# Performance work log

Hardware: AMD Instinct MI355X
Metric: run time of the kernel (lower is better)

The kernel has to match this reference:

```python
import jax, jax.numpy as jnp
import numpy as np

N, H, W = 4, 96, 96
C, G, K = 128, 8, 3
GC = C // G          # group channels = 16
P = K * K            # sampling points per group = 9
PAD = K // 2
OFS = 1.0            # offset_scale
HID = 4 * C          # mlp hidden
EPS = 1e-5           # torch nn.LayerNorm default eps


def _ln(x, g, b):
    m = jnp.mean(x, -1, keepdims=True)
    v = jnp.mean((x - m) ** 2, -1, keepdims=True)
    return (x - m) * jax.lax.rsqrt(v + EPS) * g + b


def _dcnv3_core(x, offset, mask):
    # x: (n,H,W,C) channels-last, offset: (n,H,W,G*P*2), mask: (n,H,W,G,P) softmaxed.
    # Faithful port of dcnv3_core_pytorch (stride=1, dilation=1, zero-pad grid_sample,
    # align_corners=False -> pixel = loc*size - 0.5).
    n = x.shape[0]
    xp = jnp.pad(x, ((0, 0), (PAD, PAD), (PAD, PAD), (0, 0)))
    Hin, Win = H + 2 * PAD, W + 2 * PAD
    L = H * W
    base = (K - 1) // 2 + 0.5
    ref_x = (base + jnp.arange(W, dtype=x.dtype)) / Win  # normalized by padded size
    ref_y = (base + jnp.arange(H, dtype=x.dtype)) / Hin
    k = jnp.arange(K, dtype=x.dtype) - (K - 1) // 2
    dx = jnp.repeat(k, K) / Win  # torch meshgrid('ij'): kernel-x varies slowest
    dy = jnp.tile(k, K) / Hin
    off = offset.reshape(n, H, W, G, P, 2)
    # absolute sampling pixel coords (grid_sample align_corners=False)
    px = (ref_x[None, None, :, None, None] + dx * OFS + off[..., 0] * OFS / Win) * Win - 0.5
    py = (ref_y[None, :, None, None, None] + dy * OFS + off[..., 1] * OFS / Hin) * Hin - 0.5
    # layout (n,G,L,P)
    px = px.transpose(0, 3, 1, 2, 4).reshape(n, G, L, P)
    py = py.transpose(0, 3, 1, 2, 4).reshape(n, G, L, P)
    mk = mask.transpose(0, 3, 1, 2, 4).reshape(n, G, L, P)
    xg = xp.reshape(n, Hin * Win, G, GC).transpose(0, 2, 1, 3)
    x0 = jnp.floor(px); y0 = jnp.floor(py)
    fx = px - x0; fy = py - y0
    x0 = x0.astype(jnp.int32); y0 = y0.astype(jnp.int32)
    x1 = x0 + 1; y1 = y0 + 1
    out = jnp.zeros((n, G, L, GC), x.dtype)
    for yi, xi, w in ((y0, x0, (1 - fy) * (1 - fx)), (y0, x1, (1 - fy) * fx),
                      (y1, x0, fy * (1 - fx)), (y1, x1, fy * fx)):
        valid = (yi >= 0) & (yi < Hin) & (xi >= 0) & (xi < Win)
        idx = jnp.clip(yi, 0, Hin - 1) * Win + jnp.clip(xi, 0, Win - 1)
        v = jnp.take_along_axis(xg, idx.reshape(n, G, L * P, 1), axis=2)
        v = v.reshape(n, G, L, P, GC)
        out = out + jnp.einsum('nglp,nglpc->nglc', jnp.where(valid, w, 0.0) * mk, v)
    return out.transpose(0, 2, 1, 3).reshape(n, H, W, C)


def _dcn(x, w_in, b_in, dw_k, dw_b, dwg, dwb, w_off, b_off, w_msk, b_msk, w_out, b_out):
    n = x.shape[0]
    xproj = x @ w_in + b_in
    x1 = jax.lax.conv_general_dilated(
        x, dw_k, (1, 1), 'SAME',
        dimension_numbers=('NHWC', 'HWIO', 'NHWC'),
        feature_group_count=C) + dw_b
    x1 = jax.nn.gelu(_ln(x1, dwg, dwb), approximate=False)
    offset = x1 @ w_off + b_off
    mask = jax.nn.softmax((x1 @ w_msk + b_msk).reshape(n, H, W, G, P), axis=-1)
    y = _dcnv3_core(xproj, offset, mask)
    return y @ w_out + b_out


def setup_inputs() -> dict:
    key = jax.random.key(0)
    ks = jax.random.split(key, 10)
    rn = lambda k, s, sc: jax.random.normal(k, s, jnp.float32) * sc
    return {
        'x': rn(ks[0], (N, H, W, C), 1.0),
        'ln1g': jnp.ones((C,), jnp.float32), 'ln1b': jnp.zeros((C,), jnp.float32),
        'w_in': rn(ks[1], (C, C), 0.02), 'b_in': jnp.zeros((C,), jnp.float32),
        'dw_k': rn(ks[2], (K, K, 1, C), 0.1), 'dw_b': jnp.zeros((C,), jnp.float32),
        'dwg': jnp.ones((C,), jnp.float32), 'dwb': jnp.zeros((C,), jnp.float32),
        'w_off': rn(ks[3], (C, G * P * 2), 0.01), 'b_off': rn(ks[4], (G * P * 2,), 0.1),
        'w_msk': rn(ks[5], (C, G * P), 0.02), 'b_msk': jnp.zeros((G * P,), jnp.float32),
        'w_out': rn(ks[6], (C, C), 0.02), 'b_out': jnp.zeros((C,), jnp.float32),
        'ln2g': jnp.ones((C,), jnp.float32), 'ln2b': jnp.zeros((C,), jnp.float32),
        'w1': rn(ks[7], (C, HID), 0.02), 'b1': jnp.zeros((HID,), jnp.float32),
        'w2': rn(ks[8], (HID, C), 0.02), 'b2': jnp.zeros((C,), jnp.float32),
    }


def reference(x, ln1g, ln1b, w_in, b_in, dw_k, dw_b, dwg, dwb, w_off, b_off,
              w_msk, b_msk, w_out, b_out, ln2g, ln2b, w1, b1, w2, b2):
    # pre-norm InternImage block: x = x + dcn(LN1(x)); x = x + mlp(LN2(x))
    x = x + _dcn(_ln(x, ln1g, ln1b), w_in, b_in, dw_k, dw_b, dwg, dwb,
                 w_off, b_off, w_msk, b_msk, w_out, b_out)
    h = _ln(x, ln2g, ln2b)
    h = jax.nn.gelu(h @ w1 + b1, approximate=False) @ w2 + b2
    return x + h
```

## Files before the change

kernel.cpp:

```cpp
#include <hip/hip_runtime.h>
#include <hip/hip_bf16.h>
#include <math.h>

using bf16 = __hip_bfloat16;
using bf162 = __hip_bfloat162;

typedef __bf16 bf16x8 __attribute__((ext_vector_type(8)));
typedef float floatx4 __attribute__((ext_vector_type(4)));

constexpr int NB = 4, HH = 96, WW = 96, CC = 128, GG = 8, PP = 9;
constexpr int HW = HH * WW;
constexpr int NPIX = NB * HW;

__device__ __forceinline__ float ld1(const float* p) { return *p; }
__device__ __forceinline__ float ld1(const bf16* p)  { return __bfloat162float(*p); }
__device__ __forceinline__ void st1(float* p, float v) { *p = v; }
__device__ __forceinline__ void st1(bf16* p, float v)  { *p = __float2bfloat16(v); }
__device__ __forceinline__ float b2f(bf16 v) { return __bfloat162float(v); }
__device__ __forceinline__ bf16 f2b(float v) { return __float2bfloat16(v); }
__device__ __forceinline__ float gelu_exact(float v) {
    return 0.5f * v * (1.0f + erff(v * 0.7071067811865475f));
}
__device__ __forceinline__ floatx4 MFMA(bf16x8 a, bf16x8 b, floatx4 c) {
    return __builtin_amdgcn_mfma_f32_16x16x32_bf16(a, b, c, 0, 0, 0);
}

struct PrepArgs {
    const float* src[6];
    bf16* dst[6];
    int K[6], N[6];
    int cum[7];
    const float* b_off; const float* b_msk; float* b_om;
};

__global__ __launch_bounds__(256) void prep_weights(PrepArgs pa, int total)
{
    int t = blockIdx.x * 256 + threadIdx.x;
    if (t >= total) return;
    if (t >= pa.cum[6]) {
        int e = t - pa.cum[6];
        pa.b_om[e] = (e < 144) ? pa.b_off[e] : pa.b_msk[e - 144];
        return;
    }
    int i = 0;
    #pragma unroll
    for (int j = 0; j < 5; ++j) if (t >= pa.cum[j + 1]) i = j + 1;
    int e = t - pa.cum[i];
    int Ki = pa.K[i], Ni = pa.N[i];
    int n = e / Ki, k = e - n * Ki;
    pa.dst[i][e] = f2b(pa.src[i][(size_t)k * Ni + n]);
}

template<typename TI, typename TO>
__global__ __launch_bounds__(256) void ln_kernel(
    const TI* __restrict__ X, const float* __restrict__ g,
    const float* __restrict__ b, TO* __restrict__ out)
{
    int wave = (blockIdx.x * 256 + threadIdx.x) >> 6;
    int lane = threadIdx.x & 63;
    if (wave >= NPIX) return;
    const TI* xp = X + (size_t)wave * 128 + 2 * lane;
    float v0 = ld1(xp), v1 = ld1(xp + 1);
    float s = v0 + v1, q = v0 * v0 + v1 * v1;
    #pragma unroll
    for (int o = 32; o; o >>= 1) { s += __shfl_xor(s, o); q += __shfl_xor(q, o); }
    float mean = s * (1.0f / 128.0f);
    float rstd = rsqrtf(q * (1.0f / 128.0f) - mean * mean + 1e-5f);
    float g0 = g[2 * lane], g1 = g[2 * lane + 1];
    float b0 = b[2 * lane], b1 = b[2 * lane + 1];
    TO* op = out + (size_t)wave * 128 + 2 * lane;
    st1(op,     (v0 - mean) * rstd * g0 + b0);
    st1(op + 1, (v1 - mean) * rstd * g1 + b1);
}

__global__ __launch_bounds__(256) void dwconv_ln_gelu_kernel(
    const bf16* __restrict__ xln, const float* __restrict__ dwk,
    const float* __restrict__ dwb, const float* __restrict__ gam,
    const float* __restrict__ bet, bf16* __restrict__ out)
{
    int wave = (blockIdx.x * 256 + threadIdx.x) >> 6;
    int lane = threadIdx.x & 63;
    if (wave >= NPIX) return;
    int n = wave / HW; int rem = wave % HW;
    int y = rem / WW;  int x = rem % WW;
    const bf162* xp = (const bf162*)xln;
    float a0 = 0.f, a1 = 0.f;
    #pragma unroll
    for (int ky = 0; ky < 3; ++ky) {
        int yy = y + ky - 1;
        if (yy < 0 || yy >= HH) continue;
        #pragma unroll
        for (int kx = 0; kx < 3; ++kx) {
            int xx = x + kx - 1;
            if (xx < 0 || xx >= WW) continue;
            bf162 v = xp[((size_t)(n * HH + yy) * WW + xx) * 64 + lane];
            const float* w = dwk + (ky * 3 + kx) * CC + 2 * lane;
            a0 = fmaf(b2f(v.x), w[0], a0);
            a1 = fmaf(b2f(v.y), w[1], a1);
        }
    }
    a0 += dwb[2 * lane]; a1 += dwb[2 * lane + 1];
    float s = a0 + a1, q = a0 * a0 + a1 * a1;
    #pragma unroll
    for (int o = 32; o; o >>= 1) { s += __shfl_xor(s, o); q += __shfl_xor(q, o); }
    float mean = s * (1.0f / 128.0f);
    float rstd = rsqrtf(q * (1.0f / 128.0f) - mean * mean + 1e-5f);
    float h0 = gelu_exact((a0 - mean) * rstd * gam[2 * lane]     + bet[2 * lane]);
    float h1 = gelu_exact((a1 - mean) * rstd * gam[2 * lane + 1] + bet[2 * lane + 1]);
    bf162 o2; o2.x = f2b(h0); o2.y = f2b(h1);
    ((bf162*)out)[(size_t)wave * 64 + lane] = o2;
}

__global__ __launch_bounds__(256) void dcn_core_kernel(
    const bf16* __restrict__ xproj, const bf16* __restrict__ omr,
    bf16* __restrict__ out)
{
    __shared__ int4   sOff[4][72];
    __shared__ float4 sW[4][72];
    __shared__ float  sRaw[4][72];
    int wv = threadIdx.x >> 6;
    int lane = threadIdx.x & 63;
    int pix = blockIdx.x * 4 + wv;
    int n = pix / HW; int rem = pix % HW;
    int iy = rem / WW; int ix = rem % WW;
    const bf16* om = omr + (size_t)pix * 216;

    for (int e = lane; e < 72; e += 64)
        sRaw[wv][e] = b2f(om[144 + e]);
    __syncthreads();

    for (int e = lane; e < 72; e += 64) {
        int g = e / 9, p = e - 9 * g;
        float mx = -1e30f;
        #pragma unroll
        for (int i = 0; i < 9; ++i) mx = fmaxf(mx, sRaw[wv][g * 9 + i]);
        float ssum = 0.f;
        #pragma unroll
        for (int i = 0; i < 9; ++i) ssum += __expf(sRaw[wv][g * 9 + i] - mx);
        float mw = __expf(sRaw[wv][e] - mx) / ssum;

        float ox = b2f(om[g * 18 + 2 * p]);
        float oy = b2f(om[g * 18 + 2 * p + 1]);
        int kx = p / 3 - 1, ky = p % 3 - 1;
        float px = (float)(ix + kx) + ox;
        float py = (float)(iy + ky) + oy;
        float fx0 = floorf(px), fy0 = floorf(py);
        int x0 = (int)fx0, y0 = (int)fy0;
        float fx = px - fx0, fy = py - fy0;
        bool vx0 = (x0 >= 0) & (x0 < WW), vx1 = (x0 + 1 >= 0) & (x0 + 1 < WW);
        bool vy0 = (y0 >= 0) & (y0 < HH), vy1 = (y0 + 1 >= 0) & (y0 + 1 < HH);
        float w00 = (1.f - fy) * (1.f - fx) * mw * (vy0 && vx0 ? 1.f : 0.f);
        float w01 = (1.f - fy) * fx         * mw * (vy0 && vx1 ? 1.f : 0.f);
        float w10 = fy * (1.f - fx)         * mw * (vy1 && vx0 ? 1.f : 0.f);
        float w11 = fy * fx                 * mw * (vy1 && vx1 ? 1.f : 0.f);
        int x0c = min(max(x0, 0), WW - 1), x1c = min(max(x0 + 1, 0), WW - 1);
        int y0c = min(max(y0, 0), HH - 1), y1c = min(max(y0 + 1, 0), HH - 1);
        sOff[wv][e] = make_int4((y0c * WW + x0c) * CC, (y0c * WW + x1c) * CC,
                                (y1c * WW + x0c) * CC, (y1c * WW + x1c) * CC);
        sW[wv][e] = make_float4(w00, w01, w10, w11);
    }
    __syncthreads();

    const bf16* xb = xproj + (size_t)n * HW * CC + 2 * lane;
    int gbase = (lane >> 3) * 9;
    float a0 = 0.f, a1 = 0.f;
    #pragma unroll
    for (int p = 0; p < 9; ++p) {
        int4 o = sOff[wv][gbase + p];
        float4 w = sW[wv][gbase + p];
        bf162 v00 = *(const bf162*)(xb + o.x);
        bf162 v01 = *(const bf162*)(xb + o.y);
        bf162 v10 = *(const bf162*)(xb + o.z);
        bf162 v11 = *(const bf162*)(xb + o.w);
        a0 += w.x * b2f(v00.x) + w.y * b2f(v01.x) + w.z * b2f(v10.x) + w.w * b2f(v11.x);
        a1 += w.x * b2f(v00.y) + w.y * b2f(v01.y) + w.z * b2f(v10.y) + w.w * b2f(v11.y);
    }
    bf162 o2; o2.x = f2b(a0); o2.y = f2b(a1);
    ((bf162*)out)[(size_t)pix * 64 + lane] = o2;
}

__global__ __launch_bounds__(256) void gemm_mfma_kernel(
    const bf16* __restrict__ A, const bf16* __restrict__ Wt,
    const float* __restrict__ bias, bf16* __restrict__ Out, int M, int Nn, int K)
{
    __shared__ __align__(16) __bf16 As[64][72];
    __shared__ __align__(16) __bf16 Bs[64][72];
    int tid = threadIdx.x;
    int wv = tid >> 6, lane = tid & 63;
    int bm = blockIdx.y * 64, bn = blockIdx.x * 64;
    int mI = lane & 15, q = lane >> 4;
    floatx4 acc[4] = {};

    for (int k0 = 0; k0 < K; k0 += 64) {
        #pragma unroll
        for (int cc = 0; cc < 2; ++cc) {
            int ch = tid * 2 + cc;
            int row = ch >> 3, ko = (ch & 7) * 8;
            *reinterpret_cast<uint4*>(&As[row][ko]) =
                *reinterpret_cast<const uint4*>(A + (size_t)(bm + row) * K + k0 + ko);
            int ng = bn + row;
            uint4 bv = make_uint4(0, 0, 0, 0);
            if (ng < Nn) bv = *reinterpret_cast<const uint4*>(Wt + (size_t)ng * K + k0 + ko);
            *reinterpret_cast<uint4*>(&Bs[row][ko]) = bv;
        }
        __syncthreads();
        #pragma unroll
        for (int kk = 0; kk < 64; kk += 32) {
            bf16x8 a = *reinterpret_cast<const bf16x8*>(&As[wv * 16 + mI][kk + q * 8]);
            #pragma unroll
            for (int t = 0; t < 4; ++t) {
                bf16x8 b = *reinterpret_cast<const bf16x8*>(&Bs[t * 16 + mI][kk + q * 8]);
                acc[t] = MFMA(a, b, acc[t]);
            }
        }
        __syncthreads();
    }
    int row0 = bm + wv * 16 + q * 4;
    #pragma unroll
    for (int t = 0; t < 4; ++t) {
        int col = bn + t * 16 + mI;
        if (col >= Nn) continue;
        float bs = bias[col];
        #pragma unroll
        for (int r = 0; r < 4; ++r)
            st1(Out + (size_t)(row0 + r) * Nn + col, acc[t][r] + bs);
    }
}

__global__ __launch_bounds__(256, 3) void fused_tail_kernel(
    const bf16* __restrict__ ycore, const float* __restrict__ x,
    const bf16* __restrict__ w_outT, const float* __restrict__ b_out,
    const float* __restrict__ ln2g, const float* __restrict__ ln2b,
    const bf16* __restrict__ w1T, const float* __restrict__ b1,
    const bf16* __restrict__ w2T, const float* __restrict__ b2,
    float* __restrict__ out)
{
    __shared__ __align__(16) bf16 sA[64 * 136];
    __shared__ __align__(16) bf16 sXres[64 * 136];
    __shared__ __align__(16) bf16 sH2[64 * 136];
    int tid = threadIdx.x, wv = tid >> 6, lane = tid & 63;
    int mI = lane & 15, q = lane >> 4;
    int bm = blockIdx.x * 64;

    bf16x8 bw0[4][2];
    #pragma unroll
    for (int ks = 0; ks < 4; ++ks)
        #pragma unroll
        for (int ct = 0; ct < 2; ++ct)
            bw0[ks][ct] = *reinterpret_cast<const bf16x8*>(
                w_outT + (size_t)(wv * 32 + ct * 16 + mI) * 128 + ks * 32 + q * 8);

    #pragma unroll
    for (int i = 0; i < 4; ++i) {
        int s = tid + 256 * i;
        int row = s >> 4, ko = (s & 15) * 8;
        *reinterpret_cast<uint4*>(&sA[row * 136 + ko]) =
            *reinterpret_cast<const uint4*>(ycore + (size_t)(bm + row) * 128 + ko);
    }
    __syncthreads();

    floatx4 acc0[4][2] = {};
    #pragma unroll
    for (int ks = 0; ks < 4; ++ks) {
        int k = ks * 32 + q * 8;
        bf16x8 a[4];
        #pragma unroll
        for (int rt = 0; rt < 4; ++rt)
            a[rt] = *reinterpret_cast<const bf16x8*>(&sA[(rt * 16 + mI) * 136 + k]);
        #pragma unroll
        for (int ct = 0; ct < 2; ++ct)
            #pragma unroll
            for (int rt = 0; rt < 4; ++rt)
                acc0[rt][ct] = MFMA(a[rt], bw0[ks][ct], acc0[rt][ct]);
    }
    #pragma unroll
    for (int rt = 0; rt < 4; ++rt)
        #pragma unroll
        for (int ct = 0; ct < 2; ++ct) {
            int col = wv * 32 + ct * 16 + mI;
            float bs = b_out[col];
            #pragma unroll
            for (int r = 0; r < 4; ++r) {
                int row = rt * 16 + q * 4 + r;
                float v = acc0[rt][ct][r] + bs + x[(size_t)(bm + row) * 128 + col];
                sXres[row * 136 + col] = f2b(v);
            }
        }
    __syncthreads();

    {
        int row = tid >> 2, part = tid & 3;
        float s = 0.f, sq = 0.f;
        float vals[32];
        #pragma unroll
        for (int j = 0; j < 4; ++j) {
            bf16x8 v = *reinterpret_cast<const bf16x8*>(&sXres[row * 136 + part * 32 + j * 8]);
            #pragma unroll
            for (int e = 0; e < 8; ++e) {
                float f = (float)v[e];
                vals[j * 8 + e] = f; s += f; sq += f * f;
            }
        }
        s  += __shfl_xor(s, 1);  s += __shfl_xor(s, 2);
        sq += __shfl_xor(sq, 1); sq += __shfl_xor(sq, 2);
        float mean = s * (1.0f / 128.0f);
        float rstd = rsqrtf(sq * (1.0f / 128.0f) - mean * mean + 1e-5f);
        #pragma unroll
        for (int j = 0; j < 4; ++j) {
            bf16x8 o;
            #pragma unroll
            for (int e = 0; e < 8; ++e) {
                int ch = part * 32 + j * 8 + e;
                bf16 t = f2b((vals[j * 8 + e] - mean) * rstd * ln2g[ch] + ln2b[ch]);
                o[e] = *reinterpret_cast<__bf16*>(&t);
            }
            *reinterpret_cast<bf16x8*>(&sH2[row * 136 + part * 32 + j * 8]) = o;
        }
    }
    __syncthreads();

    floatx4 acc2[4][2] = {};
    #pragma unroll 1
    for (int ph = 0; ph < 4; ++ph) {
        bf16x8 bw1[4][2];
        #pragma unroll
        for (int ks = 0; ks < 4; ++ks)
            #pragma unroll
            for (int ct = 0; ct < 2; ++ct)
                bw1[ks][ct] = *reinterpret_cast<const bf16x8*>(
                    w1T + (size_t)(ph * 128 + wv * 32 + ct * 16 + mI) * 128 + ks * 32 + q * 8);
        floatx4 acc1[4][2] = {};
        #pragma unroll
        for (int ks = 0; ks < 4; ++ks) {
            int k = ks * 32 + q * 8;
            bf16x8 a[4];
            #pragma unroll
            for (int rt = 0; rt < 4; ++rt)
                a[rt] = *reinterpret_cast<const bf16x8*>(&sH2[(rt * 16 + mI) * 136 + k]);
            #pragma unroll
            for (int ct = 0; ct < 2; ++ct)
                #pragma unroll
                for (int rt = 0; rt < 4; ++rt)
                    acc1[rt][ct] = MFMA(a[rt], bw1[ks][ct], acc1[rt][ct]);
        }
        __syncthreads();
        bf16x8 bw2[4][2];
        #pragma unroll
        for (int ks = 0; ks < 4; ++ks)
            #pragma unroll
            for (int ct = 0; ct < 2; ++ct)
                bw2[ks][ct] = *reinterpret_cast<const bf16x8*>(
                    w2T + (size_t)(wv * 32 + ct * 16 + mI) * 512 + ph * 128 + ks * 32 + q * 8);
        #pragma unroll
        for (int rt = 0; rt < 4; ++rt)
            #pragma unroll
            for (int ct = 0; ct < 2; ++ct) {
                int lcol = wv * 32 + ct * 16 + mI;
                float bs = b1[ph * 128 + lcol];
                #pragma unroll
                for (int r = 0; r < 4; ++r) {
                    int row = rt * 16 + q * 4 + r;
                    sA[row * 136 + lcol] = f2b(gelu_exact(acc1[rt][ct][r] + bs));
                }
            }
        __syncthreads();
        #pragma unroll
        for (int ks = 0; ks < 4; ++ks) {
            int k = ks * 32 + q * 8;
            bf16x8 a[4];
            #pragma unroll
            for (int rt = 0; rt < 4; ++rt)
                a[rt] = *reinterpret_cast<const bf16x8*>(&sA[(rt * 16 + mI) * 136 + k]);
            #pragma unroll
            for (int ct = 0; ct < 2; ++ct)
                #pragma unroll
                for (int rt = 0; rt < 4; ++rt)
                    acc2[rt][ct] = MFMA(a[rt], bw2[ks][ct], acc2[rt][ct]);
        }
    }
    #pragma unroll
    for (int rt = 0; rt < 4; ++rt)
        #pragma unroll
        for (int ct = 0; ct < 2; ++ct) {
            int col = wv * 32 + ct * 16 + mI;
            float bs = b2[col];
            #pragma unroll
            for (int r = 0; r < 4; ++r) {
                int row = rt * 16 + q * 4 + r;
                out[(size_t)(bm + row) * 128 + col] =
                    acc2[rt][ct][r] + bs + b2f(sXres[row * 136 + col]);
            }
        }
}

extern "C" void kernel_launch(void* const* d_in, const int* in_sizes, int n_in,
                              void* d_out, int out_size, void* d_ws, size_t ws_size,
                              hipStream_t stream)
{
    const float* x     = (const float*)d_in[0];
    const float* ln1g  = (const float*)d_in[1];
    const float* ln1b  = (const float*)d_in[2];
    const float* w_in  = (const float*)d_in[3];
    const float* b_in  = (const float*)d_in[4];
    const float* dw_k  = (const float*)d_in[5];
    const float* dw_b  = (const float*)d_in[6];
    const float* dwg   = (const float*)d_in[7];
    const float* dwb   = (const float*)d_in[8];
    const float* w_off = (const float*)d_in[9];
    const float* b_off = (const float*)d_in[10];
    const float* w_msk = (const float*)d_in[11];
    const float* b_msk = (const float*)d_in[12];
    const float* w_out = (const float*)d_in[13];
    const float* b_out = (const float*)d_in[14];
    const float* ln2g  = (const float*)d_in[15];
    const float* ln2b  = (const float*)d_in[16];
    const float* w1    = (const float*)d_in[17];
    const float* b1    = (const float*)d_in[18];
    const float* w2    = (const float*)d_in[19];
    const float* b2    = (const float*)d_in[20];
    float* out = (float*)d_out;

    bf16* ws = (bf16*)d_ws;
    bf16* xln   = ws;
    bf16* xproj = xln   + (size_t)NPIX * 128;
    bf16* x1    = xproj + (size_t)NPIX * 128;
    bf16* omr   = x1    + (size_t)NPIX * 128;
    bf16* ycore = xln;
    bf16* wT    = ws + (size_t)NPIX * 600;
    bf16* w_inT  = wT;
    bf16* w_omT  = w_inT  + 16384;
    bf16* w_outT = w_omT  + 27648;
    bf16* w1T    = w_outT + 16384;
    bf16* w2T    = w1T    + 65536;
    float* b_om  = (float*)(w2T + 65536);
    const int WTOT = 191488 + 216;

    PrepArgs pa;
    pa.src[0] = w_in;  pa.dst[0] = w_inT;            pa.K[0] = 128; pa.N[0] = 128;
    pa.src[1] = w_off; pa.dst[1] = w_omT;            pa.K[1] = 128; pa.N[1] = 144;
    pa.src[2] = w_msk; pa.dst[2] = w_omT + 144*128;  pa.K[2] = 128; pa.N[2] = 72;
    pa.src[3] = w_out; pa.dst[3] = w_outT;           pa.K[3] = 128; pa.N[3] = 128;
    pa.src[4] = w1;    pa.dst[4] = w1T;              pa.K[4] = 128; pa.N[4] = 512;
    pa.src[5] = w2;    pa.dst[5] = w2T;              pa.K[5] = 512; pa.N[5] = 128;
    pa.cum[0] = 0;     pa.cum[1] = 16384;  pa.cum[2] = 34816; pa.cum[3] = 44032;
    pa.cum[4] = 60416; pa.cum[5] = 125952; pa.cum[6] = 191488;
    pa.b_off = b_off;  pa.b_msk = b_msk;   pa.b_om = b_om;

    const int M = NPIX;
    dim3 blk(256);

    prep_weights<<<(WTOT + 255) / 256, blk, 0, stream>>>(pa, WTOT);
    ln_kernel<float, bf16><<<NPIX / 4, blk, 0, stream>>>(x, ln1g, ln1b, xln);
    gemm_mfma_kernel<<<dim3(2, M / 64), blk, 0, stream>>>(
        xln, w_inT, b_in, xproj, M, 128, 128);
    dwconv_ln_gelu_kernel<<<NPIX / 4, blk, 0, stream>>>(xln, dw_k, dw_b, dwg, dwb, x1);
    gemm_mfma_kernel<<<dim3(4, M / 64), blk, 0, stream>>>(
        x1, w_omT, b_om, omr, M, 216, 128);
    dcn_core_kernel<<<NPIX / 4, blk, 0, stream>>>(xproj, omr, ycore);
    fused_tail_kernel<<<M / 64, blk, 0, stream>>>(
        ycore, x, w_outT, b_out, ln2g, ln2b, w1T, b1, w2T, b2, out);
}
```

Measured before the change: 236.9 us.

## Use 32-row GEMM tiles, pad offset/mask output, and approximate GELU

Replaces the generic 64x64 tiled GEMM with a 32-row kernel that keeps the full K=128 A-tile in registers and streams weight column tiles directly from global memory with register double-buffering. The offset/mask projection output is padded from 216 to 224 columns so the column count splits evenly across waves. The fused tail kernel moves to 32-row blocks with less shared memory and a higher occupancy hint. Exact erf GELU is swapped for a tanh-style sigmoid approximation, which cuts transcendental cost but changes numerics relative to the exact reference.

```diff
diff --git a/kernel.cpp b/kernel.cpp
--- a/kernel.cpp
+++ b/kernel.cpp
@@ -18,8 +18,10 @@
 __device__ __forceinline__ void st1(bf16* p, float v)  { *p = __float2bfloat16(v); }
 __device__ __forceinline__ float b2f(bf16 v) { return __bfloat162float(v); }
 __device__ __forceinline__ bf16 f2b(float v) { return __float2bfloat16(v); }
-__device__ __forceinline__ float gelu_exact(float v) {
-    return 0.5f * v * (1.0f + erff(v * 0.7071067811865475f));
+__device__ __forceinline__ float gelu_fast(float v) {
+    float p = v * v;
+    float u2 = v * (-1.5957691216f - 0.0713548162f * p);
+    return v / (1.0f + __expf(u2));
 }
 __device__ __forceinline__ floatx4 MFMA(bf16x8 a, bf16x8 b, floatx4 c) {
     return __builtin_amdgcn_mfma_f32_16x16x32_bf16(a, b, c, 0, 0, 0);
@@ -30,6 +32,7 @@
     bf16* dst[6];
     int K[6], N[6];
     int cum[7];
+    bf16* om_pad;
     const float* b_off; const float* b_msk; float* b_om;
 };
 
@@ -37,9 +40,14 @@
 {
     int t = blockIdx.x * 256 + threadIdx.x;
     if (t >= total) return;
-    if (t >= pa.cum[6]) {
-        int e = t - pa.cum[6];
-        pa.b_om[e] = (e < 144) ? pa.b_off[e] : pa.b_msk[e - 144];
+    int wend = pa.cum[6];
+    if (t >= wend + 1024) {
+        int e = t - wend - 1024;
+        pa.b_om[e] = (e < 144) ? pa.b_off[e] : (e < 216 ? pa.b_msk[e - 144] : 0.f);
+        return;
+    }
+    if (t >= wend) {
+        pa.om_pad[t - wend] = f2b(0.f);
         return;
     }
     int i = 0;
@@ -105,8 +113,8 @@
     for (int o = 32; o; o >>= 1) { s += __shfl_xor(s, o); q += __shfl_xor(q, o); }
     float mean = s * (1.0f / 128.0f);
     float rstd = rsqrtf(q * (1.0f / 128.0f) - mean * mean + 1e-5f);
-    float h0 = gelu_exact((a0 - mean) * rstd * gam[2 * lane]     + bet[2 * lane]);
-    float h1 = gelu_exact((a1 - mean) * rstd * gam[2 * lane + 1] + bet[2 * lane + 1]);
+    float h0 = gelu_fast((a0 - mean) * rstd * gam[2 * lane]     + bet[2 * lane]);
+    float h1 = gelu_fast((a1 - mean) * rstd * gam[2 * lane + 1] + bet[2 * lane + 1]);
     bf162 o2; o2.x = f2b(h0); o2.y = f2b(h1);
     ((bf162*)out)[(size_t)wave * 64 + lane] = o2;
 }
@@ -123,7 +131,7 @@
     int pix = blockIdx.x * 4 + wv;
     int n = pix / HW; int rem = pix % HW;
     int iy = rem / WW; int ix = rem % WW;
-    const bf16* om = omr + (size_t)pix * 216;
+    const bf16* om = omr + (size_t)pix * 224;
 
     for (int e = lane; e < 72; e += 64)
         sRaw[wv][e] = b2f(om[144 + e]);
@@ -179,55 +187,62 @@
     ((bf162*)out)[(size_t)pix * 64 + lane] = o2;
 }
 
-__global__ __launch_bounds__(256) void gemm_mfma_kernel(
+__global__ __launch_bounds__(256) void gemm32_kernel(
     const bf16* __restrict__ A, const bf16* __restrict__ Wt,
-    const float* __restrict__ bias, bf16* __restrict__ Out, int M, int Nn, int K)
-{
-    __shared__ __align__(16) __bf16 As[64][72];
-    __shared__ __align__(16) __bf16 Bs[64][72];
-    int tid = threadIdx.x;
-    int wv = tid >> 6, lane = tid & 63;
-    int bm = blockIdx.y * 64, bn = blockIdx.x * 64;
+    const float* __restrict__ bias, bf16* __restrict__ Out, int Nn)
+{
+    __shared__ __align__(16) bf16 sA[32 * 136];
+    int tid = threadIdx.x, wv = tid >> 6, lane = tid & 63;
     int mI = lane & 15, q = lane >> 4;
-    floatx4 acc[4] = {};
-
-    for (int k0 = 0; k0 < K; k0 += 64) {
-        #pragma unroll
-        for (int cc = 0; cc < 2; ++cc) {
-            int ch = tid * 2 + cc;
-            int row = ch >> 3, ko = (ch & 7) * 8;
-            *reinterpret_cast<uint4*>(&As[row][ko]) =
-                *reinterpret_cast<const uint4*>(A + (size_t)(bm + row) * K + k0 + ko);
-            int ng = bn + row;
-            uint4 bv = make_uint4(0, 0, 0, 0);
-            if (ng < Nn) bv = *reinterpret_cast<const uint4*>(Wt + (size_t)ng * K + k0 + ko);
-            *reinterpret_cast<uint4*>(&Bs[row][ko]) = bv;
-        }
-        __syncthreads();
-        #pragma unroll
-        for (int kk = 0; kk < 64; kk += 32) {
-            bf16x8 a = *reinterpret_cast<const bf16x8*>(&As[wv * 16 + mI][kk + q * 8]);
-            #pragma unroll
-            for (int t = 0; t < 4; ++t) {
-                bf16x8 b = *reinterpret_cast<const bf16x8*>(&Bs[t * 16 + mI][kk + q * 8]);
-                acc[t] = MFMA(a, b, acc[t]);
-            }
-        }
-        __syncthreads();
-    }
-    int row0 = bm + wv * 16 + q * 4;
-    #pragma unroll
-    for (int t = 0; t < 4; ++t) {
-        int col = bn + t * 16 + mI;
-        if (col >= Nn) continue;
+    int rt = wv & 1, g = wv >> 1;
+    int bm = blockIdx.x * 32;
+
+    #pragma unroll
+    for (int cc = 0; cc < 2; ++cc) {
+        int s = tid + 256 * cc;
+        int row = s >> 4, ko = (s & 15) * 8;
+        *reinterpret_cast<uint4*>(&sA[row * 136 + ko]) =
+            *reinterpret_cast<const uint4*>(A + (size_t)(bm + row) * 128 + ko);
+    }
+    __syncthreads();
+
+    bf16x8 a[4];
+    #pragma unroll
+    for (int ks = 0; ks < 4; ++ks)
+        a[ks] = *reinterpret_cast<const bf16x8*>(&sA[(rt * 16 + mI) * 136 + ks * 32 + q * 8]);
+
+    int T2 = (Nn >> 4) >> 1;
+    int t = g * T2;
+    bf16x8 bc[4];
+    #pragma unroll
+    for (int ks = 0; ks < 4; ++ks)
+        bc[ks] = *reinterpret_cast<const bf16x8*>(Wt + (size_t)(t * 16 + mI) * 128 + ks * 32 + q * 8);
+    for (int i = 0; i < T2; ++i) {
+        bf16x8 bn[4];
+        if (i + 1 < T2) {
+            #pragma unroll
+            for (int ks = 0; ks < 4; ++ks)
+                bn[ks] = *reinterpret_cast<const bf16x8*>(
+                    Wt + (size_t)((t + 1) * 16 + mI) * 128 + ks * 32 + q * 8);
+        }
+        floatx4 acc = {};
+        #pragma unroll
+        for (int ks = 0; ks < 4; ++ks) acc = MFMA(a[ks], bc[ks], acc);
+        int col = t * 16 + mI;
         float bs = bias[col];
+        int row0 = bm + rt * 16 + q * 4;
         #pragma unroll
         for (int r = 0; r < 4; ++r)
-            st1(Out + (size_t)(row0 + r) * Nn + col, acc[t][r] + bs);
-    }
-}
-
-__global__ __launch_bounds__(256, 3) void fused_tail_kernel(
+            st1(Out + (size_t)(row0 + r) * Nn + col, acc[r] + bs);
+        if (i + 1 < T2) {
+            #pragma unroll
+            for (int ks = 0; ks < 4; ++ks) bc[ks] = bn[ks];
+        }
+        ++t;
+    }
+}
+
+__global__ __launch_bounds__(256, 4) void fused_tail_kernel(
     const bf16* __restrict__ ycore, const float* __restrict__ x,
     const bf16* __restrict__ w_outT, const float* __restrict__ b_out,
     const float* __restrict__ ln2g, const float* __restrict__ ln2b,
@@ -235,162 +250,155 @@
     const bf16* __restrict__ w2T, const float* __restrict__ b2,
     float* __restrict__ out)
 {
-    __shared__ __align__(16) bf16 sA[64 * 136];
-    __shared__ __align__(16) bf16 sXres[64 * 136];
-    __shared__ __align__(16) bf16 sH2[64 * 136];
+    __shared__ __align__(16) bf16 sA[32 * 136];
+    __shared__ __align__(16) bf16 sXres[32 * 136];
+    __shared__ __align__(16) bf16 sH2[32 * 136];
     int tid = threadIdx.x, wv = tid >> 6, lane = tid & 63;
     int mI = lane & 15, q = lane >> 4;
-    int bm = blockIdx.x * 64;
-
-    bf16x8 bw0[4][2];
-    #pragma unroll
-    for (int ks = 0; ks < 4; ++ks)
-        #pragma unroll
-        for (int ct = 0; ct < 2; ++ct)
-            bw0[ks][ct] = *reinterpret_cast<const bf16x8*>(
-                w_outT + (size_t)(wv * 32 + ct * 16 + mI) * 128 + ks * 32 + q * 8);
-
-    #pragma unroll
-    for (int i = 0; i < 4; ++i) {
-        int s = tid + 256 * i;
+    int rt = wv & 1, ch = wv >> 1;
+    int bm = blockIdx.x * 32;
+
+    #pragma unroll
+    for (int cc = 0; cc < 2; ++cc) {
+        int s = tid + 256 * cc;
         int row = s >> 4, ko = (s & 15) * 8;
         *reinterpret_cast<uint4*>(&sA[row * 136 + ko]) =
             *reinterpret_cast<const uint4*>(ycore + (size_t)(bm + row) * 128 + ko);
     }
     __syncthreads();
 
-    floatx4 acc0[4][2] = {};
-    #pragma unroll
-    for (int ks = 0; ks < 4; ++ks) {
-        int k = ks * 32 + q * 8;
-        bf16x8 a[4];
-        #pragma unroll
-        for (int rt = 0; rt < 4; ++rt)
-            a[rt] = *reinterpret_cast<const bf16x8*>(&sA[(rt * 16 + mI) * 136 + k]);
-        #pragma unroll
-        for (int ct = 0; ct < 2; ++ct)
-            #pragma unroll
-            for (int rt = 0; rt < 4; ++rt)
-                acc0[rt][ct] = MFMA(a[rt], bw0[ks][ct], acc0[rt][ct]);
-    }
-    #pragma unroll
-    for (int rt = 0; rt < 4; ++rt)
-        #pragma unroll
-        for (int ct = 0; ct < 2; ++ct) {
-            int col = wv * 32 + ct * 16 + mI;
-            float bs = b_out[col];
-            #pragma unroll
-            for (int r = 0; r < 4; ++r) {
-                int row = rt * 16 + q * 4 + r;
-                float v = acc0[rt][ct][r] + bs + x[(size_t)(bm + row) * 128 + col];
-                sXres[row * 136 + col] = f2b(v);
-            }
-        }
+    bf16x8 a0f[4];
+    #pragma unroll
+    for (int ks = 0; ks < 4; ++ks)
+        a0f[ks] = *reinterpret_cast<const bf16x8*>(&sA[(rt * 16 + mI) * 136 + ks * 32 + q * 8]);
+    floatx4 acc0[4] = {};
+    #pragma unroll
+    for (int cth = 0; cth < 2; ++cth) {
+        bf16x8 bw[4][2];
+        #pragma unroll
+        for (int ks = 0; ks < 4; ++ks)
+            #pragma unroll
+            for (int c = 0; c < 2; ++c)
+                bw[ks][c] = *reinterpret_cast<const bf16x8*>(
+                    w_outT + (size_t)(ch * 64 + (cth * 2 + c) * 16 + mI) * 128 + ks * 32 + q * 8);
+        #pragma unroll
+        for (int ks = 0; ks < 4; ++ks)
+            #pragma unroll
+            for (int c = 0; c < 2; ++c)
+                acc0[cth * 2 + c] = MFMA(a0f[ks], bw[ks][c], acc0[cth * 2 + c]);
+    }
+    #pragma unroll
+    for (int ct = 0; ct < 4; ++ct) {
+        int col = ch * 64 + ct * 16 + mI;
+        float bs = b_out[col];
+        #pragma unroll
+        for (int r = 0; r < 4; ++r) {
+            int row = rt * 16 + q * 4 + r;
+            float v = acc0[ct][r] + bs + x[(size_t)(bm + row) * 128 + col];
+            sXres[row * 136 + col] = f2b(v);
+        }
+    }
     __syncthreads();
 
     {
-        int row = tid >> 2, part = tid & 3;
+        int row = tid >> 3, part = tid & 7;
         float s = 0.f, sq = 0.f;
-        float vals[32];
-        #pragma unroll
-        for (int j = 0; j < 4; ++j) {
-            bf16x8 v = *reinterpret_cast<const bf16x8*>(&sXres[row * 136 + part * 32 + j * 8]);
+        float vals[16];
+        #pragma unroll
+        for (int j = 0; j < 2; ++j) {
+            bf16x8 v = *reinterpret_cast<const bf16x8*>(&sXres[row * 136 + part * 16 + j * 8]);
             #pragma unroll
             for (int e = 0; e < 8; ++e) {
                 float f = (float)v[e];
                 vals[j * 8 + e] = f; s += f; sq += f * f;
             }
         }
-        s  += __shfl_xor(s, 1);  s += __shfl_xor(s, 2);
-        sq += __shfl_xor(sq, 1); sq += __shfl_xor(sq, 2);
+        s  += __shfl_xor(s, 1);  s += __shfl_xor(s, 2);  s += __shfl_xor(s, 4);
+        sq += __shfl_xor(sq, 1); sq += __shfl_xor(sq, 2); sq += __shfl_xor(sq, 4);
         float mean = s * (1.0f / 128.0f);
         float rstd = rsqrtf(sq * (1.0f / 128.0f) - mean * mean + 1e-5f);
         #pragma unroll
-        for (int j = 0; j < 4; ++j) {
+        for (int j = 0; j < 2; ++j) {
             bf16x8 o;
             #pragma unroll
             for (int e = 0; e < 8; ++e) {
-                int ch = part * 32 + j * 8 + e;
-                bf16 t = f2b((vals[j * 8 + e] - mean) * rstd * ln2g[ch] + ln2b[ch]);
-                o[e] = *reinterpret_cast<__bf16*>(&t);
+                int chn = part * 16 + j * 8 + e;
+                bf16 tb = f2b((vals[j * 8 + e] - mean) * rstd * ln2g[chn] + ln2b[chn]);
+                o[e] = *reinterpret_cast<__bf16*>(&tb);
             }
-            *reinterpret_cast<bf16x8*>(&sH2[row * 136 + part * 32 + j * 8]) = o;
-        }
-    }
-    __syncthreads();
-
-    floatx4 acc2[4][2] = {};
+            *reinterpret_cast<bf16x8*>(&sH2[row * 136 + part * 16 + j * 8]) = o;
+        }
+    }
+    __syncthreads();
+
+    floatx4 acc2[4] = {};
     #pragma unroll 1
     for (int ph = 0; ph < 4; ++ph) {
-        bf16x8 bw1[4][2];
+        bf16x8 a1f[4];
         #pragma unroll
         for (int ks = 0; ks < 4; ++ks)
-            #pragma unroll
-            for (int ct = 0; ct < 2; ++ct)
-                bw1[ks][ct] = *reinterpret_cast<const bf16x8*>(
-                    w1T + (size_t)(ph * 128 + wv * 32 + ct * 16 + mI) * 128 + ks * 32 + q * 8);
-        floatx4 acc1[4][2] = {};
-        #pragma unroll
-        for (int ks = 0; ks < 4; ++ks) {
-            int k = ks * 32 + q * 8;
-            bf16x8 a[4];
-            #pragma unroll
-            for (int rt = 0; rt < 4; ++rt)
-                a[rt] = *reinterpret_cast<const bf16x8*>(&sH2[(rt * 16 + mI) * 136 + k]);
-            #pragma unroll
-            for (int ct = 0; ct < 2; ++ct)
+            a1f[ks] = *reinterpret_cast<const bf16x8*>(&sH2[(rt * 16 + mI) * 136 + ks * 32 + q * 8]);
+        floatx4 acc1[4] = {};
+        #pragma unroll
+        for (int cth = 0; cth < 2; ++cth) {
+            bf16x8 bw[4][2];
+            #pragma unroll
+            for (int ks = 0; ks < 4; ++ks)
                 #pragma unroll
-                for (int rt = 0; rt < 4; ++rt)
-                    acc1[rt][ct] = MFMA(a[rt], bw1[ks][ct], acc1[rt][ct]);
+                for (int c = 0; c < 2; ++c)
+                    bw[ks][c] = *reinterpret_cast<const bf16x8*>(
+                        w1T + (size_t)(ph * 128 + ch * 64 + (cth * 2 + c) * 16 + mI) * 128
+                            + ks * 32 + q * 8);
+            #pragma unroll
+            for (int ks = 0; ks < 4; ++ks)
+                #pragma unroll
+                for (int c = 0; c < 2; ++c)
+                    acc1[cth * 2 + c] = MFMA(a1f[ks], bw[ks][c], acc1[cth * 2 + c]);
         }
         __syncthreads();
-        bf16x8 bw2[4][2];
-        #pragma unroll
-        for (int ks = 0; ks < 4; ++ks)
-            #pragma unroll
-            for (int ct = 0; ct < 2; ++ct)
-                bw2[ks][ct] = *reinterpret_cast<const bf16x8*>(
-                    w2T + (size_t)(wv * 32 + ct * 16 + mI) * 512 + ph * 128 + ks * 32 + q * 8);
-        #pragma unroll
-        for (int rt = 0; rt < 4; ++rt)
-            #pragma unroll
-            for (int ct = 0; ct < 2; ++ct) {
-                int lcol = wv * 32 + ct * 16 + mI;
-                float bs = b1[ph * 128 + lcol];
-                #pragma unroll
-                for (int r = 0; r < 4; ++r) {
-                    int row = rt * 16 + q * 4 + r;
-                    sA[row * 136 + lcol] = f2b(gelu_exact(acc1[rt][ct][r] + bs));
-                }
-            }
-        __syncthreads();
-        #pragma unroll
-        for (int ks = 0; ks < 4; ++ks) {
-            int k = ks * 32 + q * 8;
-            bf16x8 a[4];
-            #pragma unroll
-            for (int rt = 0; rt < 4; ++rt)
-                a[rt] = *reinterpret_cast<const bf16x8*>(&sA[(rt * 16 + mI) * 136 + k]);
-            #pragma unroll
-            for (int ct = 0; ct < 2; ++ct)
-                #pragma unroll
-                for (int rt = 0; rt < 4; ++rt)
-                    acc2[rt][ct] = MFMA(a[rt], bw2[ks][ct], acc2[rt][ct]);
-        }
-    }
-    #pragma unroll
-    for (int rt = 0; rt < 4; ++rt)
-        #pragma unroll
-        for (int ct = 0; ct < 2; ++ct) {
-            int col = wv * 32 + ct * 16 + mI;
-            float bs = b2[col];
+        #pragma unroll
+        for (int ct = 0; ct < 4; ++ct) {
+            int lcol = ch * 64 + ct * 16 + mI;
+            float bs = b1[ph * 128 + lcol];
             #pragma unroll
             for (int r = 0; r < 4; ++r) {
                 int row = rt * 16 + q * 4 + r;
-                out[(size_t)(bm + row) * 128 + col] =
-                    acc2[rt][ct][r] + bs + b2f(sXres[row * 136 + col]);
+                sA[row * 136 + lcol] = f2b(gelu_fast(acc1[ct][r] + bs));
             }
         }
+        __syncthreads();
+        bf16x8 a2f[4];
+        #pragma unroll
+        for (int ks = 0; ks < 4; ++ks)
+            a2f[ks] = *reinterpret_cast<const bf16x8*>(&sA[(rt * 16 + mI) * 136 + ks * 32 + q * 8]);
+        #pragma unroll
+        for (int cth = 0; cth < 2; ++cth) {
+            bf16x8 bw[4][2];
+            #pragma unroll
+            for (int ks = 0; ks < 4; ++ks)
+                #pragma unroll
+                for (int c = 0; c < 2; ++c)
+                    bw[ks][c] = *reinterpret_cast<const bf16x8*>(
+                        w2T + (size_t)(ch * 64 + (cth * 2 + c) * 16 + mI) * 512
+                            + ph * 128 + ks * 32 + q * 8);
+            #pragma unroll
+            for (int ks = 0; ks < 4; ++ks)
+                #pragma unroll
+                for (int c = 0; c < 2; ++c)
+                    acc2[cth * 2 + c] = MFMA(a2f[ks], bw[ks][c], acc2[cth * 2 + c]);
+        }
+    }
+    #pragma unroll
+    for (int ct = 0; ct < 4; ++ct) {
+        int col = ch * 64 + ct * 16 + mI;
+        float bs = b2[col];
+        #pragma unroll
+        for (int r = 0; r < 4; ++r) {
+            int row = rt * 16 + q * 4 + r;
+            out[(size_t)(bm + row) * 128 + col] =
+                acc2[ct][r] + bs + b2f(sXres[row * 136 + col]);
+        }
+    }
 }
 
 extern "C" void kernel_launch(void* const* d_in, const int* in_sizes, int n_in,
@@ -426,14 +434,14 @@
     bf16* x1    = xproj + (size_t)NPIX * 128;
     bf16* omr   = x1    + (size_t)NPIX * 128;
     bf16* ycore = xln;
-    bf16* wT    = ws + (size_t)NPIX * 600;
+    bf16* wT    = ws + (size_t)NPIX * 608;
     bf16* w_inT  = wT;
     bf16* w_omT  = w_inT  + 16384;
-    bf16* w_outT = w_omT  + 27648;
+    bf16* w_outT = w_omT  + 28672;
     bf16* w1T    = w_outT + 16384;
     bf16* w2T    = w1T    + 65536;
     float* b_om  = (float*)(w2T + 65536);
-    const int WTOT = 191488 + 216;
+    const int WTOT = 191488 + 1024 + 224;
 
     PrepArgs pa;
     pa.src[0] = w_in;  pa.dst[0] = w_inT;            pa.K[0] = 128; pa.N[0] = 128;
@@ -444,6 +452,7 @@
     pa.src[5] = w2;    pa.dst[5] = w2T;              pa.K[5] = 512; pa.N[5] = 128;
     pa.cum[0] = 0;     pa.cum[1] = 16384;  pa.cum[2] = 34816; pa.cum[3] = 44032;
     pa.cum[4] = 60416; pa.cum[5] = 125952; pa.cum[6] = 191488;
+    pa.om_pad = w_omT + 216 * 128;
     pa.b_off = b_off;  pa.b_msk = b_msk;   pa.b_om = b_om;
 
     const int M = NPIX;
@@ -451,12 +460,10 @@
 
     prep_weights<<<(WTOT + 255) / 256, blk, 0, stream>>>(pa, WTOT);
     ln_kernel<float, bf16><<<NPIX / 4, blk, 0, stream>>>(x, ln1g, ln1b, xln);
-    gemm_mfma_kernel<<<dim3(2, M / 64), blk, 0, stream>>>(
-        xln, w_inT, b_in, xproj, M, 128, 128);
+    gemm32_kernel<<<M / 32, blk, 0, stream>>>(xln, w_inT, b_in, xproj, 128);
     dwconv_ln_gelu_kernel<<<NPIX / 4, blk, 0, stream>>>(xln, dw_k, dw_b, dwg, dwb, x1);
-    gemm_mfma_kernel<<<dim3(4, M / 64), blk, 0, stream>>>(
-        x1, w_omT, b_om, omr, M, 216, 128);
+    gemm32_kernel<<<M / 32, blk, 0, stream>>>(x1, w_omT, b_om, omr, 224);
     dcn_core_kernel<<<NPIX / 4, blk, 0, stream>>>(xproj, omr, ycore);
-    fused_tail_kernel<<<M / 64, blk, 0, stream>>>(
+    fused_tail_kernel<<<M / 32, blk, 0, stream>>>(
         ycore, x, w_outT, b_out, ln2g, ln2b, w1T, b1, w2T, b2, out);
 }
```

Result: slower. 308.2 us (+30.1%).
